# Kernel optimization log

Measured on AMD Instinct MI355X. Metric: run time of the kernel, lower is better.

## Reference

```python
import jax, jax.numpy as jnp
import numpy as np
from jax import lax

IMG_H, IMG_W = 1024, 1536
N_IMG = 8
STRIDES = [4, 8, 16, 32, 64]
SIZES = [32, 64, 128, 256, 512]
RATIOS = np.array([0.5, 1.0, 2.0], dtype=np.float64)
A = 3
PRE_NMS_TOP_N = 1000
POST_NMS_TOP_N = 1000
NMS_THRESH = 0.7
SCORE_THRESH = 0.0
MIN_SIZE = 1e-3
BBOX_CLIP = float(np.log(1000.0 / 16.0))  # torchvision BoxCoder clamp on dw/dh
FEAT_SHAPES = [(IMG_H // s, IMG_W // s) for s in STRIDES]
NUM_PER_LEVEL = [h * w * A for h, w in FEAT_SHAPES]


def _make_anchors():
    # torchvision AnchorGenerator layout: per level, (h, w, anchor) order, matching permute_and_flatten
    out = []
    for (h, w), stride, size in zip(FEAT_SHAPES, STRIDES, SIZES):
        hr = np.sqrt(RATIOS)
        wr = 1.0 / hr
        base = np.stack([-wr * size, -hr * size, wr * size, hr * size], 1) / 2.0  # [A,4]
        sx = np.arange(w) * stride
        sy = np.arange(h) * stride
        gy, gx = np.meshgrid(sy, sx, indexing="ij")
        shifts = np.stack([gx, gy, gx, gy], -1).reshape(h, w, 1, 4)
        out.append((shifts + base.reshape(1, 1, A, 4)).reshape(-1, 4))
    return np.concatenate(out, 0).astype(np.float32)  # [T,4]


def setup_inputs() -> dict:
    key = jax.random.key(0)
    ks = jax.random.split(key, 10)
    inp = {}
    for i, (h, w) in enumerate(FEAT_SHAPES):
        inp[f"obj{i}"] = jax.random.normal(ks[i], (N_IMG, A, h, w), jnp.float32)
        inp[f"delta{i}"] = jax.random.normal(ks[5 + i], (N_IMG, A * 4, h, w), jnp.float32) * 0.5
    inp["anchors"] = jnp.asarray(_make_anchors())
    return inp


def _flatten_levels(objs, deltas):
    # permute_and_flatten: [N, A*C, H, W] -> [N, H*W*A, C]
    o_all, d_all = [], []
    for o, d in zip(objs, deltas):
        n, _, h, w = o.shape
        o_all.append(o.transpose(0, 2, 3, 1).reshape(n, -1))
        d_all.append(d.reshape(n, A, 4, h, w).transpose(0, 3, 4, 1, 2).reshape(n, -1, 4))
    return jnp.concatenate(o_all, 1), jnp.concatenate(d_all, 1)


def _decode(deltas, anchors):
    # BoxCoder(weights=(1,1,1,1)).decode
    wa = anchors[:, 2] - anchors[:, 0]
    ha = anchors[:, 3] - anchors[:, 1]
    cxa = anchors[:, 0] + 0.5 * wa
    cya = anchors[:, 1] + 0.5 * ha
    dx, dy = deltas[..., 0], deltas[..., 1]
    dw = jnp.minimum(deltas[..., 2], BBOX_CLIP)
    dh = jnp.minimum(deltas[..., 3], BBOX_CLIP)
    cx = dx * wa + cxa
    cy = dy * ha + cya
    pw = jnp.exp(dw) * wa
    ph = jnp.exp(dh) * ha
    return jnp.stack([cx - 0.5 * pw, cy - 0.5 * ph, cx + 0.5 * pw, cy + 0.5 * ph], -1)


def _box_iou(b1, b2):
    area1 = (b1[:, 2] - b1[:, 0]) * (b1[:, 3] - b1[:, 1])
    area2 = (b2[:, 2] - b2[:, 0]) * (b2[:, 3] - b2[:, 1])
    lt = jnp.maximum(b1[:, None, :2], b2[None, :, :2])
    rb = jnp.minimum(b1[:, None, 2:], b2[None, :, 2:])
    wh = jnp.clip(rb - lt, 0.0)
    inter = wh[..., 0] * wh[..., 1]
    return inter / (area1[:, None] + area2[None, :] - inter)


def _nms_one(boxes, nms_boxes, scores):
    # greedy NMS with fixed shapes; invalid entries carry score=-inf
    order = jnp.argsort(-scores)  # stable descending
    b, nb, s = boxes[order], nms_boxes[order], scores[order]
    iou = _box_iou(nb, nb)  # [K,K]
    k = s.shape[0]
    idxs = jnp.arange(k)
    valid = jnp.isfinite(s)

    def body(i, suppressed):
        keep_i = jnp.logical_not(suppressed[i]) & valid[i]
        return suppressed | (keep_i & (iou[i] > NMS_THRESH) & (idxs > i))

    suppressed = lax.fori_loop(0, k, body, jnp.zeros((k,), bool))
    keep = jnp.logical_not(suppressed) & valid
    sel = jnp.argsort(jnp.where(keep, 0, 1))[:POST_NMS_TOP_N]  # stable -> kept in score order
    kept = keep[sel]
    return jnp.where(kept[:, None], b[sel], 0.0), jnp.where(kept, s[sel], 0.0)


def reference(obj0, obj1, obj2, obj3, obj4, delta0, delta1, delta2, delta3, delta4, anchors):
    objs = [obj0, obj1, obj2, obj3, obj4]
    dels = [delta0, delta1, delta2, delta3, delta4]
    objectness, deltas = _flatten_levels(objs, dels)  # [N,T], [N,T,4]
    objectness = lax.stop_gradient(objectness)  # RPN detaches objectness and deltas
    deltas = lax.stop_gradient(deltas)
    proposals = _decode(deltas, anchors)  # [N,T,4]

    # per-level pre-NMS top-k, indices offset into the concatenated anchor axis
    lvl_full = jnp.concatenate([jnp.full((n,), i, jnp.int32) for i, n in enumerate(NUM_PER_LEVEL)])
    idx_parts, off = [], 0
    for n in NUM_PER_LEVEL:
        kk = min(PRE_NMS_TOP_N, n)
        _, ti = lax.top_k(objectness[:, off:off + n], kk)
        idx_parts.append(ti + off)
        off += n
    top_idx = jnp.concatenate(idx_parts, 1)  # [N,K]

    obj_sel = jnp.take_along_axis(objectness, top_idx, 1)
    boxes = jnp.take_along_axis(proposals, top_idx[..., None], 1)  # [N,K,4]
    lvl = lvl_full[top_idx]  # [N,K]
    scores = jax.nn.sigmoid(obj_sel)

    # clip to image
    x = jnp.clip(boxes[..., 0::2], 0.0, float(IMG_W))
    y = jnp.clip(boxes[..., 1::2], 0.0, float(IMG_H))
    boxes = jnp.stack([x[..., 0], y[..., 0], x[..., 1], y[..., 1]], -1)

    # remove_small_boxes + score threshold, as -inf score masking (fixed shapes)
    ok = ((boxes[..., 2] - boxes[..., 0]) >= MIN_SIZE) & ((boxes[..., 3] - boxes[..., 1]) >= MIN_SIZE)
    ok = ok & (scores >= SCORE_THRESH)
    scores_m = jnp.where(ok, scores, -jnp.inf)

    # batched_nms trick: shift boxes by level so different levels never overlap
    offset = lvl.astype(boxes.dtype) * (max(IMG_H, IMG_W) + 1.0)
    nms_boxes = boxes + offset[..., None]

    out_boxes, _ = jax.vmap(_nms_one)(boxes, nms_boxes, scores_m)
    return out_boxes  # [N_IMG, POST_NMS_TOP_N, 4], zero-padded
```

## Files before the change

### kernel.cpp

```cpp
#include <hip/hip_runtime.h>
#include <stdint.h>

#define N_IMGS 8
#define NLVL 5
#define TOT 392832
#define PRE_K 1000
#define POST_K 1000
#define KSEL 5000
#define MASKW 79
#define MROWS 5056
#define NCHUNK 79
#define LPAD 1024
#define MSLOTS (NLVL * LPAD)
#define HCOPY 4100
#define CANDMAX 4096
#define SLICE 16384
#define NSLICE 27
#define NWS (N_IMGS * NSLICE * 4)
#define GH_U32 (N_IMGS * NLVL * 4096)

typedef unsigned long long u64;

struct Ptrs {
    const float* obj[5];
    const float* del[5];
    const float* anch;
};

__device__ __forceinline__ unsigned flipb(unsigned u) {
    return (u & 0x80000000u) ? ~u : (u | 0x80000000u);
}

__device__ __forceinline__ void lvl_info(int t, int& l, int& off, int& W, int& H) {
    if (t < 294912)      { l = 0; off = 0;      W = 384; H = 256; }
    else if (t < 368640) { l = 1; off = 294912; W = 192; H = 128; }
    else if (t < 387072) { l = 2; off = 368640; W = 96;  H = 64;  }
    else if (t < 391680) { l = 3; off = 387072; W = 48;  H = 32;  }
    else                 { l = 4; off = 391680; W = 24;  H = 16;  }
}

__device__ __forceinline__ void slice_info(int s, int& l, int& sl) {
    if (s < 18)      { l = 0; sl = s; }
    else if (s < 23) { l = 1; sl = s - 18; }
    else if (s < 25) { l = 2; sl = s - 23; }
    else if (s < 26) { l = 3; sl = s - 25; }
    else             { l = 4; sl = s - 26; }
}

__device__ __forceinline__ void lvl_consts(int l, int& len, int& off, int& HW) {
    switch (l) {
    case 0: len = 294912; off = 0;      HW = 98304; break;
    case 1: len = 73728;  off = 294912; HW = 24576; break;
    case 2: len = 18432;  off = 368640; HW = 6144;  break;
    case 3: len = 4608;   off = 387072; HW = 1536;  break;
    default: len = 1152;  off = 391680; HW = 384;   break;
    }
}

__device__ __forceinline__ void lvl_slices(int l, int& sbase, int& nsl) {
    switch (l) {
    case 0: sbase = 0;  nsl = 18; break;
    case 1: sbase = 18; nsl = 5;  break;
    case 2: sbase = 23; nsl = 2;  break;
    case 3: sbase = 25; nsl = 1;  break;
    default: sbase = 26; nsl = 1; break;
    }
}

__device__ void decode_one(const Ptrs& P, int n, int t, float bx[4], bool& valid, int& lvl) {
#pragma clang fp contract(off)
    int l, off, W, H;
    lvl_info(t, l, off, W, H);
    lvl = l;
    int i = t - off;
    int a = i % 3;
    int p = i / 3;
    int y = p / W, x = p - y * W;
    const float* D = P.del[l];
    size_t plane = (size_t)W * H;
    size_t base = ((size_t)n * 12 + (size_t)a * 4) * plane + (size_t)y * W + x;
    float dx = D[base];
    float dy = D[base + plane];
    float dw = D[base + 2 * plane];
    float dh = D[base + 3 * plane];
    const float* an = P.anch + (size_t)t * 4;
    float a0 = an[0], a1 = an[1], a2 = an[2], a3 = an[3];
    float wa = a2 - a0, ha = a3 - a1;
    float cxa = a0 + 0.5f * wa, cya = a1 + 0.5f * ha;
    const float CLIP = 4.135166556742356f;
    dw = fminf(dw, CLIP);
    dh = fminf(dh, CLIP);
    float cx = dx * wa + cxa;
    float cy = dy * ha + cya;
    float pw = expf(dw) * wa;
    float ph = expf(dh) * ha;
    float x1 = cx - 0.5f * pw, y1 = cy - 0.5f * ph;
    float x2 = cx + 0.5f * pw, y2 = cy + 0.5f * ph;
    x1 = fminf(fmaxf(x1, 0.f), 1536.f);
    x2 = fminf(fmaxf(x2, 0.f), 1536.f);
    y1 = fminf(fmaxf(y1, 0.f), 1024.f);
    y2 = fminf(fmaxf(y2, 0.f), 1024.f);
    bx[0] = x1; bx[1] = y1; bx[2] = x2; bx[3] = y2;
    valid = ((x2 - x1) >= 1e-3f) && ((y2 - y1) >= 1e-3f);
}

__global__ void k_zero_out(float* out, int n) {
    int i = blockIdx.x * blockDim.x + threadIdx.x;
    if (i < n) out[i] = 0.f;
}

__global__ void k_zero32(unsigned* p, int n) {
    int i = blockIdx.x * blockDim.x + threadIdx.x;
    if (i < n) p[i] = 0u;
}

__global__ __launch_bounds__(256) void k_hist(Ptrs P, unsigned* ghist) {
    int img = blockIdx.x / NSLICE, s = blockIdx.x % NSLICE;
    int l, sl; slice_info(s, l, sl);
    int len, off, HW; lvl_consts(l, len, off, HW);
    int start = sl * SLICE;
    int cnt4 = min(SLICE, len - start) >> 2;
    const uint4* S4 = (const uint4*)(P.obj[l] + (size_t)img * 3 * HW + start);
    __shared__ unsigned hist[2 * HCOPY];
    int t = threadIdx.x;
    for (int i = t; i < 2 * HCOPY; i += 256) hist[i] = 0u;
    __syncthreads();
    unsigned* myh = hist + (t & 1) * HCOPY;
    for (int i = t; i < cnt4; i += 256) {
        uint4 v = S4[i];
        atomicAdd(&myh[flipb(v.x) >> 20], 1u);
        atomicAdd(&myh[flipb(v.y) >> 20], 1u);
        atomicAdd(&myh[flipb(v.z) >> 20], 1u);
        atomicAdd(&myh[flipb(v.w) >> 20], 1u);
    }
    __syncthreads();
    unsigned* G = ghist + (size_t)(img * 5 + l) * 4096;
    for (int b = t; b < 4096; b += 256) {
        unsigned v = hist[b] + hist[HCOPY + b];
        if (v) atomicAdd(&G[b], v);
    }
}

__global__ __launch_bounds__(1024) void k_pivot(const unsigned* ghist, uint2* pivinfo,
                                                int* vcnt) {
    int task = blockIdx.x;
    int t = threadIdx.x;
    if (task == 0 && t < N_IMGS) vcnt[t] = KSEL;
    __shared__ unsigned hl[4096];
    __shared__ unsigned suf[1024];
    const unsigned* H = ghist + (size_t)task * 4096;
    for (int i = t; i < 4096; i += 1024) hl[i] = H[i];
    __syncthreads();
    suf[t] = hl[4 * t] + hl[4 * t + 1] + hl[4 * t + 2] + hl[4 * t + 3];
    for (int d = 1; d < 1024; d <<= 1) {
        __syncthreads();
        unsigned v = (t + d < 1024) ? suf[t + d] : 0u;
        __syncthreads();
        suf[t] += v;
    }
    __syncthreads();
    unsigned above = (t == 1023) ? 0u : suf[t + 1];
    if (suf[t] >= PRE_K && above < PRE_K) {
        int b = 4 * t + 3;
        unsigned c = above;
        while (c + hl[b] < PRE_K) { c += hl[b]; --b; }
        pivinfo[task] = make_uint2((unsigned)b, PRE_K - c);
    }
}

__global__ __launch_bounds__(256) void k_cnt(Ptrs P, const uint2* pivinfo,
                                             unsigned* cntgt, unsigned* cnteq) {
    int img = blockIdx.x / NSLICE, s = blockIdx.x % NSLICE;
    int l, sl; slice_info(s, l, sl);
    int len, off, HW; lvl_consts(l, len, off, HW);
    int start = sl * SLICE;
    int cnt4 = min(SLICE, len - start) >> 2;
    int task = img * 5 + l;
    unsigned pivot = pivinfo[task].x;
    const uint4* S4 = (const uint4*)(P.obj[l] + (size_t)img * 3 * HW + start);
    int t = threadIdx.x, lane = t & 63, wv = t >> 6;
    unsigned cg = 0u, ce = 0u;
    for (int i = t; i < cnt4; i += 256) {
        uint4 v = S4[i];
        unsigned vv[4] = {v.x, v.y, v.z, v.w};
#pragma unroll
        for (int q = 0; q < 4; ++q) {
            unsigned b = flipb(vv[q]) >> 20;
            cg += (b > pivot);
            ce += (b == pivot);
        }
    }
    for (int d = 1; d < 64; d <<= 1) {
        cg += (unsigned)__shfl_xor((int)cg, d, 64);
        ce += (unsigned)__shfl_xor((int)ce, d, 64);
    }
    if (lane == 0) {
        int ws = blockIdx.x * 4 + wv;
        cntgt[ws] = cg;
        cnteq[ws] = ce;
    }
}

__global__ __launch_bounds__(128) void k_off(const unsigned* cntgt, const unsigned* cnteq,
                                             unsigned* basegt, unsigned* baseeq, int* nc) {
    int task = blockIdx.x;
    int img = task / 5, l = task % 5;
    int sbase, nsl; lvl_slices(l, sbase, nsl);
    int nws = nsl * 4;
    int wsbase = (img * NSLICE + sbase) * 4;
    __shared__ unsigned sg[128], se[128];
    int t = threadIdx.x;
    unsigned g0 = (t < nws) ? cntgt[wsbase + t] : 0u;
    unsigned e0 = (t < nws) ? cnteq[wsbase + t] : 0u;
    sg[t] = g0; se[t] = e0;
    for (int d = 1; d < 128; d <<= 1) {
        __syncthreads();
        unsigned ag = (t >= d) ? sg[t - d] : 0u;
        unsigned ae = (t >= d) ? se[t - d] : 0u;
        __syncthreads();
        sg[t] += ag; se[t] += ae;
    }
    __syncthreads();
    if (t < nws) {
        basegt[wsbase + t] = sg[t] - g0;
        baseeq[wsbase + t] = se[t] - e0;
    }
    if (t == 0) nc[task] = (int)se[127];
}

__global__ __launch_bounds__(256) void k_write(Ptrs P, const uint2* pivinfo,
                                               const unsigned* basegt, const unsigned* baseeq,
                                               uint2* sel, u64* cand) {
    int img = blockIdx.x / NSLICE, s = blockIdx.x % NSLICE;
    int l, sl; slice_info(s, l, sl);
    int len, off, HW; lvl_consts(l, len, off, HW);
    int start = sl * SLICE;
    int cnt4 = min(SLICE, len - start) >> 2;
    int task = img * 5 + l;
    unsigned pivot = pivinfo[task].x;
    const uint4* S4 = (const uint4*)(P.obj[l] + (size_t)img * 3 * HW + start);
    uint2* out = sel + (size_t)task * PRE_K;
    u64* cd = cand + (size_t)task * CANDMAX;
    int t = threadIdx.x, lane = t & 63, wv = t >> 6;
    int ws = blockIdx.x * 4 + wv;
    unsigned og = basegt[ws], oe = baseeq[ws];
    u64 below = (1ull << lane) - 1ull;
    int iters = (cnt4 + 255) >> 8;
    uint4 nxt = (t < cnt4) ? S4[t] : make_uint4(0u, 0u, 0u, 0u);
    for (int it = 0; it < iters; ++it) {
        int ii = it * 256 + t;
        bool live = ii < cnt4;
        uint4 cur = nxt;
        int jj = (it + 1) * 256 + t;
        if (it + 1 < iters) nxt = (jj < cnt4) ? S4[jj] : make_uint4(0u, 0u, 0u, 0u);
        unsigned vv[4] = {cur.x, cur.y, cur.z, cur.w};
#pragma unroll
        for (int q = 0; q < 4; ++q) {
            unsigned u = flipb(vv[q]);
            unsigned b = u >> 20;
            bool gt = live && (b > pivot);
            bool eq = live && (b == pivot);
            unsigned tf = 0u;
            if (gt || eq) {
                int i = start + 4 * ii + q;
                int a = i / HW, rem = i - a * HW;
                tf = (unsigned)(off + rem * 3 + a);
            }
            u64 mg = __ballot((int)gt);
            if (gt) out[og + (unsigned)__popcll(mg & below)] = make_uint2(u, tf);
            og += (unsigned)__popcll(mg);
            u64 me = __ballot((int)eq);
            if (eq) {
                unsigned slot = oe + (unsigned)__popcll(me & below);
                if (slot < CANDMAX) cd[slot] = ((u64)u << 32) | (u64)tf;
            }
            oe += (unsigned)__popcll(me);
        }
    }
}

__global__ __launch_bounds__(1024) void k_rank(const uint2* pivinfo, const u64* cand,
                                               const int* nc, uint2* sel) {
    int task = blockIdx.x;
    int t = threadIdx.x;
    int C = min(nc[task], CANDMAX);
    int krem = (int)pivinfo[task].y;
    int nbase = PRE_K - krem;
    __shared__ u64 lc[CANDMAX];
    const u64* cd = cand + (size_t)task * CANDMAX;
    for (int i = t; i < C; i += 1024) lc[i] = cd[i];
    __syncthreads();
    uint2* out = sel + (size_t)task * PRE_K;
    for (int i = t; i < C; i += 1024) {
        u64 a = lc[i];
        unsigned vi = (unsigned)(a >> 32), xi = (unsigned)a;
        int rank = 0;
        for (int j = 0; j < C; ++j) {
            u64 bj = lc[j];
            unsigned vj = (unsigned)(bj >> 32), xj = (unsigned)bj;
            rank += (vj > vi) || (vj == vi && xj < xi);
        }
        if (rank < krem) out[nbase + rank] = make_uint2(vi, xi);
    }
}

__global__ __launch_bounds__(1024) void k_sort1(Ptrs P, const uint2* sel, u64* keys2) {
    __shared__ u64 s[LPAD];
    int task = blockIdx.x;
    int n = task / 5;
    int t = threadIdx.x;
    u64 key = ~0ull;
    if (t < PRE_K) {
        uint2 sv = sel[(size_t)task * PRE_K + t];
        float bx[4]; bool valid; int lv;
        decode_one(P, n, (int)sv.y, bx, valid, lv);
        key = valid ? (((u64)(~sv.x) << 32) | (u64)sv.y)
                    : (0xFFFFFFFF00000000ull | (u64)sv.y);
    }
    s[t] = key;
    for (int k = 2; k <= LPAD; k <<= 1) {
        for (int j = k >> 1; j > 0; j >>= 1) {
            __syncthreads();
            int ixj = t ^ j;
            if (ixj > t) {
                u64 a = s[t], b = s[ixj];
                bool asc = ((t & k) == 0);
                if (asc ? (a > b) : (a < b)) { s[t] = b; s[ixj] = a; }
            }
        }
    }
    __syncthreads();
    keys2[(size_t)task * LPAD + t] = s[t];
}

__global__ void k_mergedec(Ptrs P, const u64* keys2,
                           float4* boxes, float4* nboxes, int* vcnt) {
    int idx = blockIdx.x * blockDim.x + threadIdx.x;
    if (idx >= N_IMGS * MSLOTS) return;
    int n = idx / MSLOTS, slot = idx - n * MSLOTS;
    int l = slot >> 10, p = slot & (LPAD - 1);
    const u64* base = keys2 + (size_t)n * MSLOTS;
    u64 key = base[(size_t)l * LPAD + p];
    if (key == ~0ull) return;
    int rank = p;
#pragma unroll
    for (int m = 0; m < NLVL; ++m) {
        if (m == l) continue;
        const u64* L = base + (size_t)m * LPAD;
        bool le = (m < l);
        int lo = 0, hi = LPAD;
        while (lo < hi) {
            int mid = (lo + hi) >> 1;
            u64 v = L[mid];
            bool take = le ? (v <= key) : (v < key);
            if (take) lo = mid + 1; else hi = mid;
        }
        rank += lo;
    }
    if (rank >= KSEL) return;
    int oidx = n * KSEL + rank;
    if ((key >> 32) == 0xFFFFFFFFull) {
        boxes[oidx] = make_float4(0.f, 0.f, 0.f, 0.f);
        nboxes[oidx] = make_float4(0.f, 0.f, 0.f, 0.f);
        atomicMin(&vcnt[n], rank);
        return;
    }
    int t = (int)(key & 0xFFFFFFFFull);
    float bx[4]; bool valid; int lv;
    decode_one(P, n, t, bx, valid, lv);
    boxes[oidx] = make_float4(bx[0], bx[1], bx[2], bx[3]);
    float offv = (float)lv * 1537.0f;
    nboxes[oidx] = make_float4(bx[0] + offv, bx[1] + offv, bx[2] + offv, bx[3] + offv);
}

__device__ __forceinline__ float rdlane(float v, int src) {
    return __int_as_float(__builtin_amdgcn_readlane(__float_as_int(v), src));
}
__global__ __launch_bounds__(64) void k_mask(const float4* __restrict__ nboxes,
                                             u64* __restrict__ maskT) {
#pragma clang fp contract(off)
    int rb = blockIdx.x, cs = blockIdx.y, n = blockIdx.z;
    int cb0 = cs * 2, cb1 = cb0 + 1;
    if (cb1 < rb) return;
    int lane = threadIdx.x;
    int r0 = rb * 64;
    const float4 z4 = make_float4(0.f, 0.f, 0.f, 0.f);
    const float4* B = nboxes + (size_t)n * KSEL;
    float4 rbx = (r0 + lane < KSEL) ? B[r0 + lane] : z4;
    float areaR = (rbx.z - rbx.x) * (rbx.w - rbx.y);
    float4 cA = (cb0 * 64 + lane < KSEL) ? B[cb0 * 64 + lane] : z4;
    float4 cB = (cb1 * 64 + lane < KSEL && cb1 < MASKW) ? B[cb1 * 64 + lane] : z4;
    float aCA = (cA.z - cA.x) * (cA.w - cA.y);
    float aCB = (cB.z - cB.x) * (cB.w - cB.y);
    u64 cmA = __ballot(cb0 * 64 + lane < KSEL);
    u64 cmB = __ballot(cb1 * 64 + lane < KSEL && cb1 < MASKW);
    const double MID = 0x1.666667p-1;
    u64 wA = 0ull, wB = 0ull;
#pragma unroll 4
    for (int rr = 0; rr < 64; ++rr) {
        float rx1 = rdlane(rbx.x, rr), ry1 = rdlane(rbx.y, rr);
        float rx2 = rdlane(rbx.z, rr), ry2 = rdlane(rbx.w, rr);
        float aR  = rdlane(areaR, rr);
        float wvA = fmaxf(fminf(rx2, cA.z) - fmaxf(rx1, cA.x), 0.f);
        float hvA = fmaxf(fminf(ry2, cA.w) - fmaxf(ry1, cA.y), 0.f);
        float inA = wvA * hvA;
        float unA = (aR + aCA) - inA;
        bool supA = (double)inA >= MID * (double)unA;
        float wvB = fmaxf(fminf(rx2, cB.z) - fmaxf(rx1, cB.x), 0.f);
        float hvB = fmaxf(fminf(ry2, cB.w) - fmaxf(ry1, cB.y), 0.f);
        float inB = wvB * hvB;
        float unB = (aR + aCB) - inB;
        bool supB = (double)inB >= MID * (double)unB;
        u64 a = __ballot((int)supA) & cmA;
        u64 b = __ballot((int)supB) & cmB;
        u64 dm = ~((2ull << rr) - 1ull);
        if (rb == cb0) a &= dm;
        if (rb == cb1) b &= dm;
        wA = (lane == rr) ? a : wA;
        wB = (lane == rr) ? b : wB;
    }
    if (r0 + lane < KSEL) {
        if (cb0 >= rb)
            maskT[((size_t)n * MASKW + cb0) * MROWS + r0 + lane] = wA;
        if (cb1 < MASKW)
            maskT[((size_t)n * MASKW + cb1) * MROWS + r0 + lane] = wB;
    }
}

__device__ __forceinline__ u64 bcast64(u64 v, int src) {
    unsigned lo = (unsigned)__builtin_amdgcn_readlane((int)(unsigned)v, src);
    unsigned hi = (unsigned)__builtin_amdgcn_readlane((int)(unsigned)(v >> 32), src);
    return ((u64)hi << 32) | (u64)lo;
}

__device__ __forceinline__ unsigned or_red_dpp(unsigned v) {
    v |= (unsigned)__builtin_amdgcn_update_dpp(0, (int)v, 0x111, 0xf, 0xf, true);
    v |= (unsigned)__builtin_amdgcn_update_dpp(0, (int)v, 0x112, 0xf, 0xf, true);
    v |= (unsigned)__builtin_amdgcn_update_dpp(0, (int)v, 0x114, 0xf, 0xf, true);
    v |= (unsigned)__builtin_amdgcn_update_dpp(0, (int)v, 0x118, 0xf, 0xf, true);
    v |= (unsigned)__builtin_amdgcn_update_dpp(0, (int)v, 0x142, 0xa, 0xf, false);
    v |= (unsigned)__builtin_amdgcn_update_dpp(0, (int)v, 0x143, 0xc, 0xf, false);
    return v;
}

__global__ __launch_bounds__(64, 1) void k_scan(const u64* maskT, const int* vcnt,
                                                int* keep, int* nkept) {
    __shared__ int keep_lds[1024];
    int n = blockIdx.x, lane = threadIdx.x;
    int V = vcnt[n];
    const u64* MT = maskT + (size_t)n * MASKW * MROWS;

    for (int i = lane; i < 1024; i += 64) keep_lds[i] = 0;

    int cnt = 0, cntprev = 0;
    u64 keptprev = 0ull;
    bool full = false;
    int nchunks = (V + 63) >> 6;

    u64 bulk[16];
#pragma unroll
    for (int q = 0; q < 16; ++q) bulk[q] = 0ull;
    u64 wc = MT[lane];
    u64 nc = 0ull;

    for (int c = 0; c < nchunks && !full; ++c) {
        u64 part = 0ull;
#pragma unroll
        for (int q = 0; q < 16; ++q)
            part |= (q * 64 + lane < cntprev) ? bulk[q] : 0ull;
        part |= ((keptprev >> lane) & 1ull) ? nc : 0ull;

        unsigned plo = or_red_dpp((unsigned)part);
        unsigned phi = or_red_dpp((unsigned)(part >> 32));
        u64 cur = ((u64)(unsigned)__builtin_amdgcn_readlane((int)phi, 63) << 32)
                | (u64)(unsigned)__builtin_amdgcn_readlane((int)plo, 63);

        int cntNow = cnt;
        int colN = (c + 1 < NCHUNK) ? (c + 1) : (NCHUNK - 1);
        const u64* colNp = MT + (size_t)colN * MROWS;
        {
            int kr[16];
#pragma unroll
            for (int q = 0; q < 16; ++q) kr[q] = keep_lds[q * 64 + lane];
#pragma unroll
            for (int q = 0; q < 16; ++q) bulk[q] = colNp[kr[q]];
        }
        u64 nc_next = colNp[(size_t)c * 64 + lane];
        u64 wc_next = colNp[(size_t)colN * 64 + lane];

        int base = c * 64;
        int jmax = V - base; if (jmax > 64) jmax = 64;
        u64 avail = ~cur;
        if (jmax < 64) avail &= (1ull << jmax) - 1ull;
        while (avail) {
            int j = __builtin_ctzll(avail);
            if (lane == 0) keep_lds[cnt] = base + j;
            ++cnt;
            if (cnt == POST_K) { full = true; break; }
            u64 wcj = bcast64(wc, j);
            avail &= avail - 1;
            avail &= ~wcj;
        }
        keptprev = 0ull;
        for (int i = cntNow + (int)lane; i < cnt; i += 64) {
            int r = keep_lds[i];
            keptprev |= 1ull << (r - base);
        }
        {
            unsigned klo = or_red_dpp((unsigned)keptprev);
            unsigned khi = or_red_dpp((unsigned)(keptprev >> 32));
            keptprev = ((u64)(unsigned)__builtin_amdgcn_readlane((int)khi, 63) << 32)
                     | (u64)(unsigned)__builtin_amdgcn_readlane((int)klo, 63);
        }
        cntprev = cntNow;
        wc = wc_next;
        nc = nc_next;
    }

    for (int i = lane; i < cnt; i += 64) keep[n * POST_K + i] = keep_lds[i];
    if (lane == 0) nkept[n] = cnt;
}

__global__ void k_out(const float4* boxes, const int* keep, const int* nkept, float4* out) {
    int idx = blockIdx.x * blockDim.x + threadIdx.x;
    if (idx >= N_IMGS * POST_K) return;
    int n = idx / POST_K, k = idx - n * POST_K;
    float4 v = make_float4(0.f, 0.f, 0.f, 0.f);
    if (k < nkept[n]) v = boxes[(size_t)n * KSEL + keep[n * POST_K + k]];
    out[idx] = v;
}

extern "C" void kernel_launch(void* const* d_in, const int* in_sizes, int n_in,
                              void* d_out, int out_size, void* d_ws, size_t ws_size,
                              hipStream_t stream) {
    Ptrs P;
    for (int l = 0; l < 5; ++l) {
        P.obj[l] = (const float*)d_in[2 * l];
        P.del[l] = (const float*)d_in[2 * l + 1];
    }
    P.anch = (const float*)d_in[10];

    size_t o = 0;
    auto alloc = [&](size_t bytes) {
        size_t cur = o;
        o = (o + bytes + 255) & ~(size_t)255;
        return cur;
    };
    size_t off_gh     = alloc((size_t)GH_U32 * 4);
    size_t off_cnt    = alloc((size_t)NWS * 4 * 4);
    size_t off_nc     = alloc(64 * 4);
    size_t off_piv    = alloc((size_t)N_IMGS * NLVL * 8);
    size_t off_cand   = alloc((size_t)N_IMGS * NLVL * CANDMAX * 8);
    size_t off_sel    = alloc((size_t)N_IMGS * KSEL * 8);
    size_t off_keys2  = alloc((size_t)N_IMGS * MSLOTS * 8);
    size_t off_boxes  = alloc((size_t)N_IMGS * KSEL * 16);
    size_t off_nbox   = alloc((size_t)N_IMGS * KSEL * 16);
    size_t off_mask   = alloc((size_t)N_IMGS * MASKW * MROWS * 8);
    size_t off_vcnt   = alloc(N_IMGS * 4);
    size_t off_keep   = alloc((size_t)N_IMGS * POST_K * 4);
    size_t off_nkept  = alloc(N_IMGS * 4);

    float* out = (float*)d_out;
    if (o > ws_size) {
        k_zero_out<<<(out_size + 255) / 256, 256, 0, stream>>>(out, out_size);
        return;
    }

    char* w = (char*)d_ws;
    unsigned* ghist  = (unsigned*)(w + off_gh);
    unsigned* cntgt  = (unsigned*)(w + off_cnt);
    unsigned* cnteq  = cntgt + NWS;
    unsigned* basegt = cntgt + 2 * NWS;
    unsigned* baseeq = cntgt + 3 * NWS;
    int* nc          = (int*)(w + off_nc);
    uint2* pivinfo   = (uint2*)(w + off_piv);
    u64* cand        = (u64*)(w + off_cand);
    uint2* sel       = (uint2*)(w + off_sel);
    u64* keys2       = (u64*)(w + off_keys2);
    float4* boxes    = (float4*)(w + off_boxes);
    float4* nboxes   = (float4*)(w + off_nbox);
    u64* maskT       = (u64*)(w + off_mask);
    int* vcnt        = (int*)(w + off_vcnt);
    int* keep        = (int*)(w + off_keep);
    int* nkept       = (int*)(w + off_nkept);

    k_zero32<<<(GH_U32 + 255) / 256, 256, 0, stream>>>(ghist, GH_U32);
    k_hist<<<N_IMGS * NSLICE, 256, 0, stream>>>(P, ghist);
    k_pivot<<<N_IMGS * NLVL, 1024, 0, stream>>>(ghist, pivinfo, vcnt);
    k_cnt<<<N_IMGS * NSLICE, 256, 0, stream>>>(P, pivinfo, cntgt, cnteq);
    k_off<<<N_IMGS * NLVL, 128, 0, stream>>>(cntgt, cnteq, basegt, baseeq, nc);
    k_write<<<N_IMGS * NSLICE, 256, 0, stream>>>(P, pivinfo, basegt, baseeq, sel, cand);
    k_rank<<<N_IMGS * NLVL, 1024, 0, stream>>>(pivinfo, cand, nc, sel);
    k_sort1<<<N_IMGS * NLVL, 1024, 0, stream>>>(P, sel, keys2);
    k_mergedec<<<(N_IMGS * MSLOTS + 255) / 256, 256, 0, stream>>>(P, keys2, boxes, nboxes, vcnt);
    k_mask<<<dim3(NCHUNK, (MASKW + 1) / 2, N_IMGS), 64, 0, stream>>>(nboxes, maskT);
    k_scan<<<N_IMGS, 64, 0, stream>>>(maskT, vcnt, keep, nkept);
    k_out<<<(N_IMGS * POST_K + 255) / 256, 256, 0, stream>>>((const float4*)boxes, keep, nkept, (float4*)d_out);
}
```

Baseline: 297.8 us.

## Store NMS mask row-major and accumulate removed bits per row in scan

```diff
diff --git a/kernel.cpp b/kernel.cpp
--- a/kernel.cpp
+++ b/kernel.cpp
@@ -18,6 +18,7 @@
 #define NSLICE 27
 #define NWS (N_IMGS * NSLICE * 4)
 #define GH_U32 (N_IMGS * NLVL * 4096)
+#define PEND 16
 
 typedef unsigned long long u64;
 
@@ -377,7 +378,7 @@
     return __int_as_float(__builtin_amdgcn_readlane(__float_as_int(v), src));
 }
 __global__ __launch_bounds__(64) void k_mask(const float4* __restrict__ nboxes,
-                                             u64* __restrict__ maskT) {
+                                             u64* __restrict__ mask) {
 #pragma clang fp contract(off)
     int rb = blockIdx.x, cs = blockIdx.y, n = blockIdx.z;
     int cb0 = cs * 2, cb1 = cb0 + 1;
@@ -420,10 +421,9 @@
         wB = (lane == rr) ? b : wB;
     }
     if (r0 + lane < KSEL) {
-        if (cb0 >= rb)
-            maskT[((size_t)n * MASKW + cb0) * MROWS + r0 + lane] = wA;
-        if (cb1 < MASKW)
-            maskT[((size_t)n * MASKW + cb1) * MROWS + r0 + lane] = wB;
+        size_t row = ((size_t)n * MROWS + r0 + lane) * MASKW;
+        if (cb0 >= rb) mask[row + cb0] = wA;
+        if (cb1 < MASKW) mask[row + cb1] = wB;
     }
 }
 
@@ -443,81 +443,91 @@
     return v;
 }
 
-__global__ __launch_bounds__(64, 1) void k_scan(const u64* maskT, const int* vcnt,
+__global__ __launch_bounds__(64, 1) void k_scan(const u64* mask, const int* vcnt,
                                                 int* keep, int* nkept) {
-    __shared__ int keep_lds[1024];
     int n = blockIdx.x, lane = threadIdx.x;
     int V = vcnt[n];
-    const u64* MT = maskT + (size_t)n * MASKW * MROWS;
-
-    for (int i = lane; i < 1024; i += 64) keep_lds[i] = 0;
-
-    int cnt = 0, cntprev = 0;
+    const u64* M = mask + (size_t)n * MROWS * MASKW;
+
+    u64 rem_lo = 0ull, rem_hi = 0ull;
+    u64 pl[PEND], ph[PEND];
+#pragma unroll
+    for (int q = 0; q < PEND; ++q) { pl[q] = 0ull; ph[q] = 0ull; }
+    int npend = 0;
     u64 keptprev = 0ull;
+    int prevbase = 0;
+    int cnt = 0;
     bool full = false;
     int nchunks = (V + 63) >> 6;
 
-    u64 bulk[16];
+    u64 wc = M[(size_t)lane * MASKW];
+    u64 nc = 0ull;
+
+    for (int c = 0; c < nchunks && !full; ++c) {
 #pragma unroll
-    for (int q = 0; q < 16; ++q) bulk[q] = 0ull;
-    u64 wc = MT[lane];
-    u64 nc = 0ull;
-
-    for (int c = 0; c < nchunks && !full; ++c) {
-        u64 part = 0ull;
+        for (int q = 0; q < PEND; ++q) {
+            rem_lo |= (q < npend) ? pl[q] : 0ull;
+            rem_hi |= (q < npend) ? ph[q] : 0ull;
+        }
+
+        {
+            u64 kb = keptprev;
+            int kr[PEND];
+            int nn = 0;
 #pragma unroll
-        for (int q = 0; q < 16; ++q)
-            part |= (q * 64 + lane < cntprev) ? bulk[q] : 0ull;
-        part |= ((keptprev >> lane) & 1ull) ? nc : 0ull;
-
-        unsigned plo = or_red_dpp((unsigned)part);
-        unsigned phi = or_red_dpp((unsigned)(part >> 32));
-        u64 cur = ((u64)(unsigned)__builtin_amdgcn_readlane((int)phi, 63) << 32)
-                | (u64)(unsigned)__builtin_amdgcn_readlane((int)plo, 63);
-
-        int cntNow = cnt;
+            for (int q = 0; q < PEND; ++q) {
+                if (kb) { kr[q] = prevbase + (int)__builtin_ctzll(kb); kb &= kb - 1; ++nn; }
+                else kr[q] = 0;
+            }
+#pragma unroll
+            for (int q = 0; q < PEND; ++q) {
+                const u64* row = M + (size_t)kr[q] * MASKW;
+                pl[q] = (q < nn) ? row[lane] : 0ull;
+                ph[q] = (q < nn) ? row[64 + lane] : 0ull;
+            }
+            npend = nn;
+            while (kb) {
+                int r = prevbase + (int)__builtin_ctzll(kb);
+                kb &= kb - 1;
+                const u64* row = M + (size_t)r * MASKW;
+                rem_lo |= row[lane];
+                if (lane < 15) rem_hi |= row[64 + lane];
+            }
+        }
+
+        u64 cur = bcast64((c < 64) ? rem_lo : rem_hi, c & 63);
+        {
+            u64 part = ((keptprev >> lane) & 1ull) ? nc : 0ull;
+            unsigned plo = or_red_dpp((unsigned)part);
+            unsigned phi = or_red_dpp((unsigned)(part >> 32));
+            cur |= ((u64)(unsigned)__builtin_amdgcn_readlane((int)phi, 63) << 32)
+                 | (u64)(unsigned)__builtin_amdgcn_readlane((int)plo, 63);
+        }
+
         int colN = (c + 1 < NCHUNK) ? (c + 1) : (NCHUNK - 1);
-        const u64* colNp = MT + (size_t)colN * MROWS;
-        {
-            int kr[16];
-#pragma unroll
-            for (int q = 0; q < 16; ++q) kr[q] = keep_lds[q * 64 + lane];
-#pragma unroll
-            for (int q = 0; q < 16; ++q) bulk[q] = colNp[kr[q]];
-        }
-        u64 nc_next = colNp[(size_t)c * 64 + lane];
-        u64 wc_next = colNp[(size_t)colN * 64 + lane];
+        u64 nc_next = M[((size_t)c * 64 + lane) * MASKW + colN];
+        u64 wc_next = M[((size_t)colN * 64 + lane) * MASKW + colN];
 
         int base = c * 64;
         int jmax = V - base; if (jmax > 64) jmax = 64;
         u64 avail = ~cur;
         if (jmax < 64) avail &= (1ull << jmax) - 1ull;
+        u64 keptbits = 0ull;
         while (avail) {
             int j = __builtin_ctzll(avail);
-            if (lane == 0) keep_lds[cnt] = base + j;
+            if (lane == 0) keep[n * POST_K + cnt] = base + j;
             ++cnt;
+            keptbits |= 1ull << j;
             if (cnt == POST_K) { full = true; break; }
             u64 wcj = bcast64(wc, j);
             avail &= avail - 1;
             avail &= ~wcj;
         }
-        keptprev = 0ull;
-        for (int i = cntNow + (int)lane; i < cnt; i += 64) {
-            int r = keep_lds[i];
-            keptprev |= 1ull << (r - base);
-        }
-        {
-            unsigned klo = or_red_dpp((unsigned)keptprev);
-            unsigned khi = or_red_dpp((unsigned)(keptprev >> 32));
-            keptprev = ((u64)(unsigned)__builtin_amdgcn_readlane((int)khi, 63) << 32)
-                     | (u64)(unsigned)__builtin_amdgcn_readlane((int)klo, 63);
-        }
-        cntprev = cntNow;
+        keptprev = keptbits;
+        prevbase = base;
         wc = wc_next;
         nc = nc_next;
     }
-
-    for (int i = lane; i < cnt; i += 64) keep[n * POST_K + i] = keep_lds[i];
     if (lane == 0) nkept[n] = cnt;
 }
 
@@ -555,7 +565,7 @@
     size_t off_keys2  = alloc((size_t)N_IMGS * MSLOTS * 8);
     size_t off_boxes  = alloc((size_t)N_IMGS * KSEL * 16);
     size_t off_nbox   = alloc((size_t)N_IMGS * KSEL * 16);
-    size_t off_mask   = alloc((size_t)N_IMGS * MASKW * MROWS * 8);
+    size_t off_mask   = alloc((size_t)N_IMGS * MROWS * MASKW * 8 + 1024);
     size_t off_vcnt   = alloc(N_IMGS * 4);
     size_t off_keep   = alloc((size_t)N_IMGS * POST_K * 4);
     size_t off_nkept  = alloc(N_IMGS * 4);
@@ -579,7 +589,7 @@
     u64* keys2       = (u64*)(w + off_keys2);
     float4* boxes    = (float4*)(w + off_boxes);
     float4* nboxes   = (float4*)(w + off_nbox);
-    u64* maskT       = (u64*)(w + off_mask);
+    u64* mask        = (u64*)(w + off_mask);
     int* vcnt        = (int*)(w + off_vcnt);
     int* keep        = (int*)(w + off_keep);
     int* nkept       = (int*)(w + off_nkept);
@@ -593,7 +603,7 @@
     k_rank<<<N_IMGS * NLVL, 1024, 0, stream>>>(pivinfo, cand, nc, sel);
     k_sort1<<<N_IMGS * NLVL, 1024, 0, stream>>>(P, sel, keys2);
     k_mergedec<<<(N_IMGS * MSLOTS + 255) / 256, 256, 0, stream>>>(P, keys2, boxes, nboxes, vcnt);
-    k_mask<<<dim3(NCHUNK, (MASKW + 1) / 2, N_IMGS), 64, 0, stream>>>(nboxes, maskT);
-    k_scan<<<N_IMGS, 64, 0, stream>>>(maskT, vcnt, keep, nkept);
+    k_mask<<<dim3(NCHUNK, (MASKW + 1) / 2, N_IMGS), 64, 0, stream>>>(nboxes, mask);
+    k_scan<<<N_IMGS, 64, 0, stream>>>(mask, vcnt, keep, nkept);
     k_out<<<(N_IMGS * POST_K + 255) / 256, 256, 0, stream>>>((const float4*)boxes, keep, nkept, (float4*)d_out);
 }
```

After: 543.2 us. 82.4% more time.
